# Optimization experiments

Measured on AMD Instinct MI355X. Metric: run time of the kernel, lower is better.

## Reference

```python
import jax, jax.numpy as jnp
import numpy as np

B, N, D_NODE, D_EDGE, D_GRAPH = 2, 1024, 128, 16, 128
MID, OUT = 64, 128


def _linear_params(key, fan_in, fan_out):
    # haiku Linear default: truncated-normal(stddev=1/sqrt(fan_in)) weight, zero bias
    w = jax.random.normal(key, (fan_in, fan_out), dtype=jnp.float32) / np.sqrt(fan_in)
    b = jnp.zeros((fan_out,), dtype=jnp.float32)
    return w, b


def setup_inputs() -> dict:
    key = jax.random.key(0)
    ks = jax.random.split(key, 12)
    features = jax.random.normal(ks[0], (B, N, D_NODE), dtype=jnp.float32)
    e_features = jax.random.normal(ks[1], (B, N, N, D_EDGE), dtype=jnp.float32)
    g_features = jax.random.normal(ks[2], (B, D_GRAPH), dtype=jnp.float32)
    adj = jax.random.randint(ks[3], (B, N, N), 0, 2).astype(jnp.float32)
    # ensure self-loops so every row has at least one valid neighbor
    adj = jnp.maximum(adj, jnp.eye(N, dtype=jnp.float32)[None])
    Wm, bm = _linear_params(ks[4], D_NODE, OUT)
    Wskip, bskip = _linear_params(ks[5], D_NODE, OUT)
    W1, b1 = _linear_params(ks[6], D_NODE, MID)
    W2, b2 = _linear_params(ks[7], D_NODE, MID)
    We, be = _linear_params(ks[8], D_EDGE, MID)
    Wg, bg = _linear_params(ks[9], D_GRAPH, MID)
    Wa, ba = _linear_params(ks[10], MID, 1)
    return dict(features=features, e_features=e_features, g_features=g_features,
                adj=adj, Wm=Wm, bm=bm, Wskip=Wskip, bskip=bskip,
                W1=W1, b1=b1, W2=W2, b2=b2, We=We, be=be, Wg=Wg, bg=bg,
                Wa=Wa, ba=ba)


def reference(features, e_features, g_features, adj,
              Wm, bm, Wskip, bskip, W1, b1, W2, b2, We, be, Wg, bg, Wa, ba):
    # bias mask: 0 where edge exists, -1e9 where not
    bias_mat = (adj - 1.0) * 1e9  # (b,n,n)

    values = features @ Wm + bm          # (b,n,out)
    pre_att_1 = features @ W1 + b1       # (b,n,mid) -> per-target j
    pre_att_2 = features @ W2 + b2       # (b,n,mid) -> per-source i
    pre_att_e = e_features @ We + be     # (b,n,n,mid)
    pre_att_g = g_features @ Wg + bg     # (b,mid)

    # pre_att[b,i,j] = p1[b,j] + p2[b,i] + pe[b,i,j] + pg[b]
    pre_att = (pre_att_1[:, None, :, :] + pre_att_2[:, :, None, :]
               + pre_att_e + pre_att_g[:, None, None, :])  # (b,n,n,mid)

    logits = jnp.squeeze(jax.nn.leaky_relu(pre_att) @ Wa + ba, axis=-1)  # (b,n,n)
    coefs = jax.nn.softmax(logits + bias_mat, axis=-1)                   # (b,n,n)

    ret = jnp.matmul(coefs, values)       # (b,n,out)
    ret = ret + (features @ Wskip + bskip)  # residual
    return jax.nn.relu(ret)               # activation=relu
```

## Files before the change

kernel.cpp:

```cpp
#include <hip/hip_runtime.h>
#include <hip/hip_bf16.h>
#include <cstdint>

#define B_   2
#define N_   1024
#define DN_  128
#define DE_  16
#define DG_  128
#define MID_ 64
#define OUT_ 128
#define TI_  2
#define PR_ROWS 4

typedef short bf16x8 __attribute__((ext_vector_type(8)));
typedef float f32x4  __attribute__((ext_vector_type(4)));

__device__ inline short f2bf(float f) {
    union { float f; unsigned u; } v; v.f = f;
    unsigned r = v.u + 0x7FFFu + ((v.u >> 16) & 1u);
    return (short)(unsigned short)(r >> 16);
}

__device__ inline unsigned pk2(float lo, float hi) {
    union { __hip_bfloat162 h; unsigned u; } p;
    p.h = __float22bfloat162_rn(make_float2(lo, hi));
    return p.u;
}

__global__ void __launch_bounds__(384) prep_all(
    const float* __restrict__ features, const float* __restrict__ g_features,
    const float* __restrict__ Wm, const float* __restrict__ bm,
    const float* __restrict__ Wskip, const float* __restrict__ bskip,
    const float* __restrict__ W1, const float* __restrict__ b1,
    const float* __restrict__ W2, const float* __restrict__ b2,
    const float* __restrict__ We, const float* __restrict__ be,
    const float* __restrict__ Wg, const float* __restrict__ bg,
    float* __restrict__ values, float* __restrict__ skipo,
    float* __restrict__ P1x, float* __restrict__ p2,
    float* __restrict__ pg, short* __restrict__ We_frag)
{
    const int t   = threadIdx.x;
    const int blk = blockIdx.x;

    if (blk == 512) {
        for (int e = t; e < 4 * 64 * 8; e += 384) {
            const int c    = e >> 9;
            const int lane = (e >> 3) & 63;
            const int j    = e & 7;
            const int quad = lane >> 4, s = lane & 15;
            short v = 0;
            if (quad < 2) v = f2bf(We[(quad * 8 + j) * MID_ + c * 16 + s]);
            We_frag[e] = v;
        }
        return;
    }
    if (blk == 513) {
        if (t < MID_) {
            float a0 = bg[t], a1 = bg[t];
            for (int k = 0; k < DG_; ++k) {
                const float w = Wg[k * MID_ + t];
                a0 += g_features[k] * w;
                a1 += g_features[DG_ + k] * w;
            }
            pg[t] = a0; pg[MID_ + t] = a1;
        }
        return;
    }

    const int r0 = blk * PR_ROWS;
    __shared__ float feat[PR_ROWS][DN_];
    for (int idx = t; idx < PR_ROWS * DN_; idx += 384)
        feat[idx >> 7][idx & 127] = features[(size_t)r0 * DN_ + idx];
    __syncthreads();

    const float* W; int c, stride; float base; float* outp; int ostride;
    if (t < 128) {
        W = Wm;    c = t;       stride = OUT_; base = bm[c];
        outp = values + (size_t)r0 * OUT_ + c; ostride = OUT_;
    } else if (t < 256) {
        W = Wskip; c = t - 128; stride = OUT_; base = bskip[c];
        outp = skipo + (size_t)r0 * OUT_ + c;  ostride = OUT_;
    } else if (t < 320) {
        W = W1;    c = t - 256; stride = MID_; base = b1[c] + be[c];
        outp = P1x + (size_t)r0 * MID_ + c;    ostride = MID_;
    } else {
        W = W2;    c = t - 320; stride = MID_; base = b2[c];
        outp = p2 + (size_t)r0 * MID_ + c;     ostride = MID_;
    }

    float acc[PR_ROWS] = {};
    for (int k = 0; k < DN_; ++k) {
        const float w = W[k * stride + c];
        #pragma unroll
        for (int q = 0; q < PR_ROWS; ++q) acc[q] += feat[q][k] * w;
    }
    #pragma unroll
    for (int q = 0; q < PR_ROWS; ++q) outp[q * ostride] = acc[q] + base;
}

__global__ void __launch_bounds__(256) k_logits(
    const float* __restrict__ e_features, const short* __restrict__ We_frag,
    const float* __restrict__ Wa, const float* __restrict__ P1x,
    const float* __restrict__ p2, const float* __restrict__ pg,
    float* __restrict__ lg)
{
    const int t    = threadIdx.x;
    const int wv   = t >> 6;
    const int l    = t & 63;
    const int quad = l >> 4;
    const int s    = l & 15;
    const int r    = blockIdx.x;
    const int jb   = r & 1;
    const int ri   = r >> 1;
    const int b    = ri >> 9;
    const int i0   = (ri & 511) * TI_;

    bf16x8 bfr[4];
    float  wa_r[4], p2i[TI_][4];
    #pragma unroll
    for (int c = 0; c < 4; ++c) {
        bfr[c]  = *(const bf16x8*)&We_frag[(c * 64 + l) * 8];
        wa_r[c] = Wa[c * 16 + s];
        const float pgc = pg[b * MID_ + c * 16 + s];
        #pragma unroll
        for (int ii = 0; ii < TI_; ++ii)
            p2i[ii][c] = p2[((size_t)(b * N_ + i0 + ii)) * MID_ + c * 16 + s] + pgc;
    }
    const size_t erow0 = (size_t)(b * N_ + i0) * N_;
    const int jt0 = jb * 32;

    float4 eA[TI_][2];
    if (quad < 2) {
        #pragma unroll
        for (int ii = 0; ii < TI_; ++ii) {
            const float* ep = &e_features[(erow0 + (size_t)ii * N_ + (jt0 + wv) * 16 + s) * DE_ + quad * 8];
            eA[ii][0] = *(const float4*)ep;
            eA[ii][1] = *(const float4*)(ep + 4);
        }
    }
    for (int it = 0; it < 8; ++it) {
        const int tile = jt0 + wv + it * 4;
        const int j0   = tile * 16;

        unsigned af[TI_][4];
        #pragma unroll
        for (int ii = 0; ii < TI_; ++ii) {
            if (quad < 2) {
                af[ii][0] = pk2(eA[ii][0].x, eA[ii][0].y);
                af[ii][1] = pk2(eA[ii][0].z, eA[ii][0].w);
                af[ii][2] = pk2(eA[ii][1].x, eA[ii][1].y);
                af[ii][3] = pk2(eA[ii][1].z, eA[ii][1].w);
            } else {
                af[ii][0] = af[ii][1] = af[ii][2] = af[ii][3] = 0u;
            }
        }
        if (it < 7 && quad < 2) {
            const int jn = (tile + 4) * 16;
            #pragma unroll
            for (int ii = 0; ii < TI_; ++ii) {
                const float* ep = &e_features[(erow0 + (size_t)ii * N_ + jn + s) * DE_ + quad * 8];
                eA[ii][0] = *(const float4*)ep;
                eA[ii][1] = *(const float4*)(ep + 4);
            }
        }
        float bse[4][4];
        {
            const float* pb = &P1x[((size_t)(b * N_) + j0 + quad * 4) * MID_ + s];
            #pragma unroll
            for (int c = 0; c < 4; ++c)
                #pragma unroll
                for (int rr = 0; rr < 4; ++rr)
                    bse[c][rr] = pb[rr * MID_ + c * 16];
        }
        #pragma unroll
        for (int ii = 0; ii < TI_; ++ii) {
            union { unsigned u[4]; bf16x8 v; } a;
            a.u[0] = af[ii][0]; a.u[1] = af[ii][1];
            a.u[2] = af[ii][2]; a.u[3] = af[ii][3];
            f32x4 acc[4];
            #pragma unroll
            for (int c = 0; c < 4; ++c) {
                f32x4 cin;
                cin[0] = bse[c][0] + p2i[ii][c];
                cin[1] = bse[c][1] + p2i[ii][c];
                cin[2] = bse[c][2] + p2i[ii][c];
                cin[3] = bse[c][3] + p2i[ii][c];
                acc[c] = __builtin_amdgcn_mfma_f32_16x16x32_bf16(a.v, bfr[c], cin, 0, 0, 0);
            }
            float tt[4];
            #pragma unroll
            for (int rr = 0; rr < 4; ++rr) {
                float x0 = acc[0][rr], x1 = acc[1][rr], x2 = acc[2][rr], x3 = acc[3][rr];
                x0 = fmaxf(x0, 0.01f * x0);
                x1 = fmaxf(x1, 0.01f * x1);
                x2 = fmaxf(x2, 0.01f * x2);
                x3 = fmaxf(x3, 0.01f * x3);
                tt[rr] = x0 * wa_r[0] + x1 * wa_r[1] + x2 * wa_r[2] + x3 * wa_r[3];
            }
            #pragma unroll
            for (int o = 1; o < 16; o <<= 1) {
                tt[0] += __shfl_xor(tt[0], o);
                tt[1] += __shfl_xor(tt[1], o);
                tt[2] += __shfl_xor(tt[2], o);
                tt[3] += __shfl_xor(tt[3], o);
            }
            if (s < 4)
                lg[((size_t)(b * N_ + i0 + ii)) * N_ + j0 + quad * 4 + s] = tt[s];
        }
    }
}

__global__ void __launch_bounds__(256) k_attn(
    const float* __restrict__ lg, const float* __restrict__ adj,
    const float* __restrict__ values, const float* __restrict__ skipo,
    float* __restrict__ out)
{
    const int t  = threadIdx.x;
    const int wv = t >> 6;
    const int l  = t & 63;
    const int r  = blockIdx.x;
    const int b  = (r >> 2) & 1;
    const int i0 = (((r >> 3) << 2) | (r & 3)) * TI_;

    __shared__ float lgP[TI_][N_];
    __shared__ float redv[4][16][20];
    __shared__ float sinv[TI_];
    __shared__ float pmax[4];
    __shared__ float psum[4];

    {
        const int rw = wv & 1, h = wv >> 1;
        const int c0 = h * 512 + l * 4;
        const float* lrow = &lg[(size_t)(b * N_ + i0 + rw) * N_];
        const size_t arb  = (size_t)(b * N_ + i0 + rw) * N_;
        float4 lv[2], av[2];
        #pragma unroll
        for (int q = 0; q < 2; ++q) {
            lv[q] = *(const float4*)&lrow[c0 + 256 * q];
            av[q] = *(const float4*)&adj[arb + c0 + 256 * q];
        }
        const float NEG = -3.4e38f;
        float m = NEG;
        #pragma unroll
        for (int q = 0; q < 2; ++q) {
            m = fmaxf(m, av[q].x > 0.f ? lv[q].x : NEG);
            m = fmaxf(m, av[q].y > 0.f ? lv[q].y : NEG);
            m = fmaxf(m, av[q].z > 0.f ? lv[q].z : NEG);
            m = fmaxf(m, av[q].w > 0.f ? lv[q].w : NEG);
        }
        #pragma unroll
        for (int o = 1; o < 64; o <<= 1) m = fmaxf(m, __shfl_xor(m, o));
        if (l == 0) pmax[wv] = m;
        __syncthreads();
        m = fmaxf(pmax[rw], pmax[2 + rw]);
        float sum = 0.f;
        #pragma unroll
        for (int q = 0; q < 2; ++q) {
            float4 e4;
            e4.x = av[q].x > 0.f ? __expf(lv[q].x - m) : 0.f;
            e4.y = av[q].y > 0.f ? __expf(lv[q].y - m) : 0.f;
            e4.z = av[q].z > 0.f ? __expf(lv[q].z - m) : 0.f;
            e4.w = av[q].w > 0.f ? __expf(lv[q].w - m) : 0.f;
            *(float4*)&lgP[rw][c0 + 256 * q] = e4;
            sum += (e4.x + e4.y) + (e4.z + e4.w);
        }
        #pragma unroll
        for (int o = 1; o < 64; o <<= 1) sum += __shfl_xor(sum, o);
        if (l == 0) psum[wv] = sum;
        __syncthreads();
        if (t < TI_) sinv[t] = 1.0f / (psum[t] + psum[t + 2]);
    }

    const int cg = l & 15, jp = l >> 4, ch0 = cg * 8;
    float acc[TI_][8] = {};
    const float* vb = values + (size_t)b * N_ * OUT_ + ch0;
    for (int k = 0; k < 64; ++k) {
        const int j = wv * 4 + jp + k * 16;
        float cw[TI_];
        #pragma unroll
        for (int ii = 0; ii < TI_; ++ii) cw[ii] = lgP[ii][j];
        const float* vp = vb + (size_t)j * OUT_;
        const float4 v0 = *(const float4*)vp;
        const float4 v1 = *(const float4*)(vp + 4);
        const float vv[8] = {v0.x, v0.y, v0.z, v0.w, v1.x, v1.y, v1.z, v1.w};
        #pragma unroll
        for (int ii = 0; ii < TI_; ++ii)
            #pragma unroll
            for (int kk = 0; kk < 8; ++kk)
                acc[ii][kk] += cw[ii] * vv[kk];
    }
    #pragma unroll
    for (int ii = 0; ii < TI_; ++ii)
        #pragma unroll
        for (int kk = 0; kk < 8; ++kk) {
            acc[ii][kk] += __shfl_xor(acc[ii][kk], 16);
            acc[ii][kk] += __shfl_xor(acc[ii][kk], 32);
        }
    if (l < 16) {
        #pragma unroll
        for (int ii = 0; ii < TI_; ++ii)
            #pragma unroll
            for (int q = 0; q < 2; ++q) {
                float4 w4 = make_float4(acc[ii][q * 4], acc[ii][q * 4 + 1],
                                        acc[ii][q * 4 + 2], acc[ii][q * 4 + 3]);
                *(float4*)&redv[wv][l][ii * 8 + q * 4] = w4;
            }
    }
    __syncthreads();
    {
        const int ch = t & 127, g = ch >> 3, kk = ch & 7;
        const int ii = t >> 7;
        float sum = redv[0][g][ii * 8 + kk];
        #pragma unroll
        for (int w = 1; w < 4; ++w) sum += redv[w][g][ii * 8 + kk];
        const size_t ob = ((size_t)(b * N_ + i0 + ii)) * OUT_ + ch;
        out[ob] = fmaxf(sum * sinv[ii] + skipo[ob], 0.f);
    }
}

extern "C" void kernel_launch(void* const* d_in, const int* in_sizes, int n_in,
                              void* d_out, int out_size, void* d_ws, size_t ws_size,
                              hipStream_t stream) {
    const float* features   = (const float*)d_in[0];
    const float* e_features = (const float*)d_in[1];
    const float* g_features = (const float*)d_in[2];
    const float* adj        = (const float*)d_in[3];
    const float* Wm    = (const float*)d_in[4];
    const float* bm    = (const float*)d_in[5];
    const float* Wskip = (const float*)d_in[6];
    const float* bskip = (const float*)d_in[7];
    const float* W1    = (const float*)d_in[8];
    const float* b1    = (const float*)d_in[9];
    const float* W2    = (const float*)d_in[10];
    const float* b2    = (const float*)d_in[11];
    const float* We    = (const float*)d_in[12];
    const float* be    = (const float*)d_in[13];
    const float* Wg    = (const float*)d_in[14];
    const float* bg    = (const float*)d_in[15];
    const float* Wa    = (const float*)d_in[16];
    float* out = (float*)d_out;

    float* ws      = (float*)d_ws;
    float* values  = ws;
    float* skipo   = ws + 262144;
    float* P1x     = ws + 524288;
    float* p2      = ws + 655360;
    float* pg      = ws + 786432;
    short* We_frag = (short*)(ws + 786560);
    float* lg      = ws + 787584;

    prep_all<<<B_ * N_ / PR_ROWS + 2, 384, 0, stream>>>(
        features, g_features, Wm, bm, Wskip, bskip, W1, b1, W2, b2,
        We, be, Wg, bg, values, skipo, P1x, p2, pg, We_frag);
    k_logits<<<B_ * N_ / TI_ * 2, 256, 0, stream>>>(
        e_features, We_frag, Wa, P1x, p2, pg, lg);
    k_attn<<<B_ * N_ / TI_, 256, 0, stream>>>(
        lg, adj, values, skipo, out);
}
```

Baseline: 307.3 us.

## Transpose MFMA operands, store P1 transposed, and double-buffer edge and P1 prefetch

Result: faster. 294.9 us (-4.0%).

```diff
diff --git a/kernel.cpp b/kernel.cpp
--- a/kernel.cpp
+++ b/kernel.cpp
@@ -36,7 +36,7 @@
     const float* __restrict__ We, const float* __restrict__ be,
     const float* __restrict__ Wg, const float* __restrict__ bg,
     float* __restrict__ values, float* __restrict__ skipo,
-    float* __restrict__ P1x, float* __restrict__ p2,
+    float* __restrict__ P1xT, float* __restrict__ p2,
     float* __restrict__ pg, short* __restrict__ We_frag)
 {
     const int t   = threadIdx.x;
@@ -82,7 +82,7 @@
         outp = skipo + (size_t)r0 * OUT_ + c;  ostride = OUT_;
     } else if (t < 320) {
         W = W1;    c = t - 256; stride = MID_; base = b1[c] + be[c];
-        outp = P1x + (size_t)r0 * MID_ + c;    ostride = MID_;
+        outp = P1xT + (size_t)c * (B_ * N_) + r0; ostride = 1;
     } else {
         W = W2;    c = t - 320; stride = MID_; base = b2[c];
         outp = p2 + (size_t)r0 * MID_ + c;     ostride = MID_;
@@ -100,7 +100,7 @@
 
 __global__ void __launch_bounds__(256) k_logits(
     const float* __restrict__ e_features, const short* __restrict__ We_frag,
-    const float* __restrict__ Wa, const float* __restrict__ P1x,
+    const float* __restrict__ Wa, const float* __restrict__ P1xT,
     const float* __restrict__ p2, const float* __restrict__ pg,
     float* __restrict__ lg)
 {
@@ -116,29 +116,51 @@
     const int i0   = (ri & 511) * TI_;
 
     bf16x8 bfr[4];
-    float  wa_r[4], p2i[TI_][4];
+    float  wa_l[4][4];
+    f32x4  p2l[TI_][4];
     #pragma unroll
     for (int c = 0; c < 4; ++c) {
-        bfr[c]  = *(const bf16x8*)&We_frag[(c * 64 + l) * 8];
-        wa_r[c] = Wa[c * 16 + s];
-        const float pgc = pg[b * MID_ + c * 16 + s];
-        #pragma unroll
-        for (int ii = 0; ii < TI_; ++ii)
-            p2i[ii][c] = p2[((size_t)(b * N_ + i0 + ii)) * MID_ + c * 16 + s] + pgc;
+        bfr[c] = *(const bf16x8*)&We_frag[(c * 64 + l) * 8];
+        #pragma unroll
+        for (int rr = 0; rr < 4; ++rr)
+            wa_l[c][rr] = Wa[c * 16 + quad * 4 + rr];
+        const float4 pg4 = *(const float4*)&pg[b * MID_ + c * 16 + quad * 4];
+        #pragma unroll
+        for (int ii = 0; ii < TI_; ++ii) {
+            const float4 p4 = *(const float4*)&p2[((size_t)(b * N_ + i0 + ii)) * MID_ + c * 16 + quad * 4];
+            p2l[ii][c][0] = p4.x + pg4.x;
+            p2l[ii][c][1] = p4.y + pg4.y;
+            p2l[ii][c][2] = p4.z + pg4.z;
+            p2l[ii][c][3] = p4.w + pg4.w;
+        }
     }
     const size_t erow0 = (size_t)(b * N_ + i0) * N_;
     const int jt0 = jb * 32;
-
-    float4 eA[TI_][2];
+    const float* p1b = P1xT + (size_t)(quad * 4) * (B_ * N_) + b * N_ + s;
+
+    float4 eA0[TI_][2], eA1[TI_][2];
+    float  bA[4][4], bB[4][4];
     if (quad < 2) {
         #pragma unroll
         for (int ii = 0; ii < TI_; ++ii) {
-            const float* ep = &e_features[(erow0 + (size_t)ii * N_ + (jt0 + wv) * 16 + s) * DE_ + quad * 8];
-            eA[ii][0] = *(const float4*)ep;
-            eA[ii][1] = *(const float4*)(ep + 4);
-        }
-    }
-    for (int it = 0; it < 8; ++it) {
+            const float* ep0 = &e_features[(erow0 + (size_t)ii * N_ + (jt0 + wv) * 16 + s) * DE_ + quad * 8];
+            eA0[ii][0] = *(const float4*)ep0;
+            eA0[ii][1] = *(const float4*)(ep0 + 4);
+            const float* ep1 = &e_features[(erow0 + (size_t)ii * N_ + (jt0 + wv + 4) * 16 + s) * DE_ + quad * 8];
+            eA1[ii][0] = *(const float4*)ep1;
+            eA1[ii][1] = *(const float4*)(ep1 + 4);
+        }
+    }
+    {
+        const float* pb = p1b + (jt0 + wv) * 16;
+        #pragma unroll
+        for (int c = 0; c < 4; ++c)
+            #pragma unroll
+            for (int rr = 0; rr < 4; ++rr)
+                bA[c][rr] = pb[(size_t)(c * 16 + rr) * (B_ * N_)];
+    }
+
+    auto do_tile = [&](float4 (&eAr)[TI_][2], float (&bC)[4][4], float (&bN)[4][4], int it) {
         const int tile = jt0 + wv + it * 4;
         const int j0   = tile * 16;
 
@@ -146,31 +168,29 @@
         #pragma unroll
         for (int ii = 0; ii < TI_; ++ii) {
             if (quad < 2) {
-                af[ii][0] = pk2(eA[ii][0].x, eA[ii][0].y);
-                af[ii][1] = pk2(eA[ii][0].z, eA[ii][0].w);
-                af[ii][2] = pk2(eA[ii][1].x, eA[ii][1].y);
-                af[ii][3] = pk2(eA[ii][1].z, eA[ii][1].w);
+                af[ii][0] = pk2(eAr[ii][0].x, eAr[ii][0].y);
+                af[ii][1] = pk2(eAr[ii][0].z, eAr[ii][0].w);
+                af[ii][2] = pk2(eAr[ii][1].x, eAr[ii][1].y);
+                af[ii][3] = pk2(eAr[ii][1].z, eAr[ii][1].w);
             } else {
                 af[ii][0] = af[ii][1] = af[ii][2] = af[ii][3] = 0u;
             }
         }
-        if (it < 7 && quad < 2) {
-            const int jn = (tile + 4) * 16;
+        if (it < 6 && quad < 2) {
             #pragma unroll
             for (int ii = 0; ii < TI_; ++ii) {
-                const float* ep = &e_features[(erow0 + (size_t)ii * N_ + jn + s) * DE_ + quad * 8];
-                eA[ii][0] = *(const float4*)ep;
-                eA[ii][1] = *(const float4*)(ep + 4);
+                const float* ep = &e_features[(erow0 + (size_t)ii * N_ + (size_t)(tile + 8) * 16 + s) * DE_ + quad * 8];
+                eAr[ii][0] = *(const float4*)ep;
+                eAr[ii][1] = *(const float4*)(ep + 4);
             }
         }
-        float bse[4][4];
-        {
-            const float* pb = &P1x[((size_t)(b * N_) + j0 + quad * 4) * MID_ + s];
+        if (it < 7) {
+            const float* pb = p1b + (tile + 4) * 16;
             #pragma unroll
             for (int c = 0; c < 4; ++c)
                 #pragma unroll
                 for (int rr = 0; rr < 4; ++rr)
-                    bse[c][rr] = pb[rr * MID_ + c * 16];
+                    bN[c][rr] = pb[(size_t)(c * 16 + rr) * (B_ * N_)];
         }
         #pragma unroll
         for (int ii = 0; ii < TI_; ++ii) {
@@ -179,34 +199,26 @@
             a.u[2] = af[ii][2]; a.u[3] = af[ii][3];
             f32x4 acc[4];
             #pragma unroll
-            for (int c = 0; c < 4; ++c) {
-                f32x4 cin;
-                cin[0] = bse[c][0] + p2i[ii][c];
-                cin[1] = bse[c][1] + p2i[ii][c];
-                cin[2] = bse[c][2] + p2i[ii][c];
-                cin[3] = bse[c][3] + p2i[ii][c];
-                acc[c] = __builtin_amdgcn_mfma_f32_16x16x32_bf16(a.v, bfr[c], cin, 0, 0, 0);
-            }
-            float tt[4];
-            #pragma unroll
-            for (int rr = 0; rr < 4; ++rr) {
-                float x0 = acc[0][rr], x1 = acc[1][rr], x2 = acc[2][rr], x3 = acc[3][rr];
-                x0 = fmaxf(x0, 0.01f * x0);
-                x1 = fmaxf(x1, 0.01f * x1);
-                x2 = fmaxf(x2, 0.01f * x2);
-                x3 = fmaxf(x3, 0.01f * x3);
-                tt[rr] = x0 * wa_r[0] + x1 * wa_r[1] + x2 * wa_r[2] + x3 * wa_r[3];
-            }
-            #pragma unroll
-            for (int o = 1; o < 16; o <<= 1) {
-                tt[0] += __shfl_xor(tt[0], o);
-                tt[1] += __shfl_xor(tt[1], o);
-                tt[2] += __shfl_xor(tt[2], o);
-                tt[3] += __shfl_xor(tt[3], o);
-            }
-            if (s < 4)
-                lg[((size_t)(b * N_ + i0 + ii)) * N_ + j0 + quad * 4 + s] = tt[s];
-        }
+            for (int c = 0; c < 4; ++c)
+                acc[c] = __builtin_amdgcn_mfma_f32_16x16x32_bf16(bfr[c], a.v, p2l[ii][c], 0, 0, 0);
+            float part = 0.f;
+            #pragma unroll
+            for (int c = 0; c < 4; ++c)
+                #pragma unroll
+                for (int rr = 0; rr < 4; ++rr) {
+                    float x = acc[c][rr] + bC[c][rr];
+                    x = fmaxf(x, 0.01f * x);
+                    part += x * wa_l[c][rr];
+                }
+            part += __shfl_xor(part, 16);
+            part += __shfl_xor(part, 32);
+            if (l < 16)
+                lg[((size_t)(b * N_ + i0 + ii)) * N_ + j0 + l] = part;
+        }
+    };
+    for (int it2 = 0; it2 < 8; it2 += 2) {
+        do_tile(eA0, bA, bB, it2);
+        do_tile(eA1, bB, bA, it2 + 1);
     }
 }
 
@@ -343,7 +355,7 @@
     float* ws      = (float*)d_ws;
     float* values  = ws;
     float* skipo   = ws + 262144;
-    float* P1x     = ws + 524288;
+    float* P1xT    = ws + 524288;
     float* p2      = ws + 655360;
     float* pg      = ws + 786432;
     short* We_frag = (short*)(ws + 786560);
@@ -351,9 +363,9 @@
 
     prep_all<<<B_ * N_ / PR_ROWS + 2, 384, 0, stream>>>(
         features, g_features, Wm, bm, Wskip, bskip, W1, b1, W2, b2,
-        We, be, Wg, bg, values, skipo, P1x, p2, pg, We_frag);
+        We, be, Wg, bg, values, skipo, P1xT, p2, pg, We_frag);
     k_logits<<<B_ * N_ / TI_ * 2, 256, 0, stream>>>(
-        e_features, We_frag, Wa, P1x, p2, pg, lg);
+        e_features, We_frag, Wa, P1xT, p2, pg, lg);
     k_attn<<<B_ * N_ / TI_, 256, 0, stream>>>(
         lg, adj, values, skipo, out);
 }
```
